# Kernel optimization log

Hardware: AMD Instinct MI355X
Metric: run time of the kernel (lower is better)

## Reference

```python
import jax, jax.numpy as jnp
import numpy as np

TOP_K = 2
EPS = float(np.finfo(np.float64).eps)  # combine() clamps zeros to np.finfo(float).eps


def setup_inputs() -> dict:
    key = jax.random.key(0)
    ks = jax.random.split(key, 6)
    B, D, H, O, E = 2048, 1024, 2048, 512, 8
    return {
        "x": jax.random.normal(ks[0], (B, D), dtype=jnp.float32),
        "w_gate": jax.random.normal(ks[1], (D, E), dtype=jnp.float32) * 0.02,
        "fc1_w": jax.random.normal(ks[2], (E, D, H), dtype=jnp.float32) * 0.02,
        "fc1_b": jax.random.normal(ks[3], (E, H), dtype=jnp.float32) * 0.02,
        "fc2_w": jax.random.normal(ks[4], (E, H, O), dtype=jnp.float32) * 0.02,
        "fc2_b": jax.random.normal(ks[5], (E, O), dtype=jnp.float32) * 0.02,
    }


def _gates(x, w_gate):
    # Noisy top-k gating in eval mode (no noise): clean logits -> top-k -> softmax over top-k -> scatter.
    logits = x @ w_gate                              # [B, E]
    top_logits, top_idx = jax.lax.top_k(logits, TOP_K)  # [B, K]
    top_gates = jax.nn.softmax(top_logits, axis=-1)      # 'softmax' gating over selected experts
    B = x.shape[0]
    gates = jnp.zeros(logits.shape, logits.dtype)
    gates = gates.at[jnp.arange(B)[:, None], top_idx].set(top_gates)
    return gates                                      # [B, E], zero for non-selected experts


def reference(x, w_gate, fc1_w, fc1_b, fc2_w, fc2_b):
    gates = _gates(x, w_gate)                         # [B, E]
    # Dense-equivalent of SparseDispatcher: non-selected experts have gate 0,
    # so weighting by gates reproduces dispatch/expert/combine exactly.
    h = jax.nn.gelu(jnp.einsum('bd,edh->ebh', x, fc1_w) + fc1_b[:, None, :],
                    approximate=False)                # [E, B, H]
    logp = jax.nn.log_softmax(jnp.einsum('ebh,eho->ebo', h, fc2_w) + fc2_b[:, None, :],
                              axis=-1)                # [E, B, O] (MLP ends with LogSoftmax)
    # combine: sum_e gates[b,e] * exp(logp_e[b]), clamp zeros to eps, then log
    combined = jnp.einsum('ebo,be->bo', jnp.exp(logp), gates)  # [B, O]
    combined = jnp.where(combined == 0, jnp.asarray(EPS, combined.dtype), combined)
    return jnp.log(combined)
```

## Files before the change

kernel.cpp:

```cpp
#include <hip/hip_runtime.h>
#include <stdint.h>

#define Bn 2048
#define Dn 1024
#define Hn 2048
#define On 512
#define En 8

typedef float f32x4 __attribute__((ext_vector_type(4)));
typedef unsigned short ushort_t;
typedef unsigned char u8;

__device__ __forceinline__ ushort_t f2bf(float v) {
  union { float f; uint32_t u; } a; a.f = v;
  uint32_t u = a.u;
  return (ushort_t)((u + 0x7fffu + ((u >> 16) & 1u)) >> 16);
}

__device__ __forceinline__ void gload16(const void* g, void* l) {
  __builtin_amdgcn_global_load_lds((const uint32_t*)g, (uint32_t*)l, 16, 0, 0);
}

__device__ __forceinline__ int pk4_fp8(float a, float b, float c, float d) {
  int w = __builtin_amdgcn_cvt_pk_fp8_f32(a, b, 0, false);
  w = __builtin_amdgcn_cvt_pk_fp8_f32(c, d, w, true);
  return w;
}

__device__ __forceinline__ u8 f2fp8(float v) {
  int w = __builtin_amdgcn_cvt_pk_fp8_f32(v, v, 0, false);
  return (u8)(w & 0xff);
}

__global__ void init_kernel(int* counts, int* cursors) {
  int t = threadIdx.x;
  if (t < En) { counts[t] = 0; cursors[t] = 0; }
}

__global__ __launch_bounds__(256) void cast_x8_kernel(const float* __restrict__ in,
                                                      u8* __restrict__ out) {
  int i = blockIdx.x * 256 + threadIdx.x;
  const float4* p = (const float4*)in + (size_t)i * 4;
  float4 a = p[0], b = p[1], c = p[2], d = p[3];
  int4 o;
  o.x = pk4_fp8(a.x, a.y, a.z, a.w);
  o.y = pk4_fp8(b.x, b.y, b.z, b.w);
  o.z = pk4_fp8(c.x, c.y, c.z, c.w);
  o.w = pk4_fp8(d.x, d.y, d.z, d.w);
  *(int4*)(out + (size_t)i * 16) = o;
}

#define NB_G (Bn / 8)
#define NB_T1 ((Dn / 64) * (Hn / 64) * En)
#define NB_T2 ((Hn / 64) * (On / 64) * En)
#define WSCALE 64.0f

__device__ __forceinline__ void tcast64_f8(const float* __restrict__ inp,
                                           u8* __restrict__ outp,
                                           int R, int C, int r0, int c0, float* tile) {
  int t = threadIdx.x;
  int rr = t >> 4, cc4 = (t & 15) * 4;
#pragma unroll
  for (int j = 0; j < 4; j++) {
    float4 v = *(const float4*)&inp[(size_t)(r0 + j * 16 + rr) * C + c0 + cc4];
    float* tp = &tile[(j * 16 + rr) * 65 + cc4];
    tp[0] = v.x; tp[1] = v.y; tp[2] = v.z; tp[3] = v.w;
  }
  __syncthreads();
  int orow = t >> 2, g = t & 3;
  int4 o;
#pragma unroll
  for (int q = 0; q < 4; q++) {
    float v0 = tile[(g * 16 + q * 4 + 0) * 65 + orow] * WSCALE;
    float v1 = tile[(g * 16 + q * 4 + 1) * 65 + orow] * WSCALE;
    float v2 = tile[(g * 16 + q * 4 + 2) * 65 + orow] * WSCALE;
    float v3 = tile[(g * 16 + q * 4 + 3) * 65 + orow] * WSCALE;
    ((int*)&o)[q] = pk4_fp8(v0, v1, v2, v3);
  }
  *(int4*)&outp[(size_t)(c0 + orow) * R + r0 + g * 16] = o;
}

__global__ __launch_bounds__(256) void prep_kernel(
    const float* __restrict__ x, const float* __restrict__ wg,
    const float* __restrict__ fc1w, const float* __restrict__ fc2w,
    u8* __restrict__ w1t8, u8* __restrict__ w2t8,
    int* __restrict__ top_idx, float* __restrict__ gates, int* __restrict__ counts) {
  __shared__ float smem[En * Dn];
  __shared__ int lcnt[En];
  int bid = blockIdx.x;
  int t = threadIdx.x;

  if (bid < NB_G) {
    float* wgs = smem;
    for (int i = t; i < Dn * En; i += 256) {
      int d = i >> 3, e = i & 7;
      wgs[e * Dn + d] = wg[i];
    }
    if (t < En) lcnt[t] = 0;
    __syncthreads();
    int w = t >> 6, lane = t & 63;
#pragma unroll
    for (int r = 0; r < 2; r++) {
      int b = bid * 8 + w * 2 + r;
      const float* xr = x + (size_t)b * Dn;
      float xv[16];
#pragma unroll
      for (int j = 0; j < 16; j++) xv[j] = xr[lane + j * 64];
      float acc[En];
#pragma unroll
      for (int e = 0; e < En; e++) acc[e] = 0.f;
#pragma unroll
      for (int j = 0; j < 16; j++) {
        int d = lane + j * 64;
#pragma unroll
        for (int e = 0; e < En; e++) acc[e] += xv[j] * wgs[e * Dn + d];
      }
#pragma unroll
      for (int off = 32; off; off >>= 1) {
#pragma unroll
        for (int e = 0; e < En; e++) acc[e] += __shfl_down(acc[e], off);
      }
      if (lane == 0) {
        float best = -1e30f, second = -1e30f; int bi = 0, si = 0;
#pragma unroll
        for (int e = 0; e < En; e++) {
          float l = acc[e];
          if (l > best) { second = best; si = bi; best = l; bi = e; }
          else if (l > second) { second = l; si = e; }
        }
        float e1 = expf(second - best);
        float inv = 1.f / (1.f + e1);
        top_idx[2 * b] = bi; top_idx[2 * b + 1] = si;
        gates[2 * b] = inv;  gates[2 * b + 1] = e1 * inv;
        atomicAdd(&lcnt[bi], 1);
        atomicAdd(&lcnt[si], 1);
      }
    }
    __syncthreads();
    if (t < En) {
      int c = lcnt[t];
      if (c) atomicAdd(&counts[t], c);
    }
  } else if (bid < NB_G + NB_T1) {
    int idx = bid - NB_G;
    constexpr int TPE = (Dn / 64) * (Hn / 64);
    int z = idx / TPE, rem = idx % TPE;
    int r0 = (rem / (Hn / 64)) * 64, c0 = (rem % (Hn / 64)) * 64;
    tcast64_f8(fc1w + (size_t)z * Dn * Hn, w1t8 + (size_t)z * Dn * Hn, Dn, Hn, r0, c0, smem);
  } else {
    int idx = bid - NB_G - NB_T1;
    constexpr int TPE = (Hn / 64) * (On / 64);
    int z = idx / TPE, rem = idx % TPE;
    int r0 = (rem / (On / 64)) * 64, c0 = (rem % (On / 64)) * 64;
    tcast64_f8(fc2w + (size_t)z * Hn * On, w2t8 + (size_t)z * Hn * On, Hn, On, r0, c0, smem);
  }
}

__global__ void offsets_kernel(const int* counts, int* offsets, int* cursors) {
  if (threadIdx.x == 0) {
    int s = 0;
    for (int e = 0; e < En; e++) { offsets[e] = s; s += counts[e]; }
  }
  if (threadIdx.x < En) cursors[threadIdx.x] = 0;
}

__global__ void assign_kernel(const int* __restrict__ top_idx, const int* __restrict__ offsets,
                              int* cursors, int* __restrict__ s2r, int* __restrict__ r2s) {
  int b = blockIdx.x * 256 + threadIdx.x;
  if (b >= Bn) return;
#pragma unroll
  for (int k = 0; k < 2; k++) {
    int e = top_idx[2 * b + k];
    int pos = atomicAdd(&cursors[e], 1);
    int slot = offsets[e] + pos;
    s2r[slot] = b;
    r2s[2 * b + k] = slot;
  }
}

template <bool FC1, int N, int K, int SPLITK>
__global__ __launch_bounds__(256, 8) void fp8_gemm_kernel(
    const u8* __restrict__ A, const u8* __restrict__ WT,
    const float* __restrict__ bias, const int* __restrict__ offsets,
    const int* __restrict__ counts, const int* __restrict__ s2r,
    u8* __restrict__ outH8, float* __restrict__ outL, float* __restrict__ outL2) {
  constexpr int NBL = N / 64;
  constexpr int KS = K / SPLITK;
  constexpr int NT = KS / 64;
  int e = blockIdx.z;
  int cnt = counts[e];
  int rb = blockIdx.y;
  if (rb * 64 >= cnt) return;
  int base = offsets[e];
  int ks = blockIdx.x / NBL;
  int nb = (blockIdx.x % NBL) * 64;
  int k0 = ks * KS;
  __shared__ __align__(16) u8 As[64 * 64];
  __shared__ __align__(16) u8 Bs[64 * 64];
  int t = threadIdx.x;
  int lane = t & 63, w = t >> 6;
  int wr = w >> 1, wc = w & 1;

  int srow = t >> 2;
  int sslot = (t & 3) ^ ((srow >> 1) & 3);
  int scol = sslot * 16;

  int lr = rb * 64 + srow;
  int lrc = lr < cnt ? lr : cnt - 1;
  const u8* aptr = A + (size_t)(FC1 ? s2r[base + lrc] : (base + lrc)) * K + k0 + scol;
  const u8* bptr = WT + ((size_t)e * N + nb + srow) * K + k0 + scol;

  f32x4 zero = {0.f, 0.f, 0.f, 0.f};
  f32x4 acc[2][2];
#pragma unroll
  for (int m = 0; m < 2; m++)
#pragma unroll
    for (int n = 0; n < 2; n++) acc[m][n] = zero;

  int a_r = wr * 32 + (lane & 15);
  int b_r = wc * 32 + (lane & 15);
  int rkey = ((lane & 15) >> 1) & 3;
  int slb = (lane >> 4) >> 1;
  int half = ((lane >> 4) & 1) * 8;

  for (int kt = 0; kt < NT; kt++) {
    gload16(aptr + kt * 64, &As[t * 16]);
    gload16(bptr + kt * 64, &Bs[t * 16]);
    __syncthreads();
#pragma unroll
    for (int kk = 0; kk < 2; kk++) {
      long af[2], bfr[2];
#pragma unroll
      for (int m = 0; m < 2; m++)
        af[m] = *(const long*)(As + (a_r + m * 16) * 64 +
                               (((kk * 2 + slb) ^ rkey) << 4) + half);
#pragma unroll
      for (int n = 0; n < 2; n++)
        bfr[n] = *(const long*)(Bs + (b_r + n * 16) * 64 +
                                (((kk * 2 + slb) ^ rkey) << 4) + half);
#pragma unroll
      for (int m = 0; m < 2; m++)
#pragma unroll
        for (int n = 0; n < 2; n++)
          acc[m][n] = __builtin_amdgcn_mfma_f32_16x16x32_fp8_fp8(af[m], bfr[n], acc[m][n], 0, 0, 0);
    }
    __syncthreads();
  }

  const float INV = 1.0f / WSCALE;
  float* dst = (SPLITK > 1 && ks > 0) ? outL2 : outL;
  int lr0 = rb * 64 + wr * 32;
#pragma unroll
  for (int m = 0; m < 2; m++) {
#pragma unroll
    for (int i = 0; i < 4; i++) {
      int orow = lr0 + m * 16 + (lane >> 4) * 4 + i;
      if (orow < cnt) {
        int slot = base + orow;
#pragma unroll
        for (int n = 0; n < 2; n++) {
          int col = nb + wc * 32 + n * 16 + (lane & 15);
          if (FC1) {
            float v = acc[m][n][i] * INV + bias[e * N + col];
            float g = 0.5f * v * (1.0f + erff(v * 0.70710678118654752f));
            outH8[(size_t)slot * N + col] = f2fp8(g);
          } else {
            float v = acc[m][n][i] * INV + (ks == 0 ? bias[e * N + col] : 0.f);
            dst[(size_t)slot * N + col] = v;
          }
        }
      }
    }
  }
}

__device__ __forceinline__ float blk_reduce(float v, bool ismax) {
  __shared__ float sbuf[4];
  int lane = threadIdx.x & 63, w = threadIdx.x >> 6;
#pragma unroll
  for (int off = 32; off; off >>= 1) {
    float o = __shfl_down(v, off);
    v = ismax ? fmaxf(v, o) : (v + o);
  }
  __syncthreads();
  if (lane == 0) sbuf[w] = v;
  __syncthreads();
  float r = sbuf[0];
#pragma unroll
  for (int i = 1; i < 4; i++) r = ismax ? fmaxf(r, sbuf[i]) : (r + sbuf[i]);
  return r;
}

__global__ void combine_kernel(const float* __restrict__ l2a, const float* __restrict__ l2b,
                               const int* __restrict__ r2s, const float* __restrict__ gates,
                               float* __restrict__ out) {
  int b = blockIdx.x, t = threadIdx.x;
  float c0 = 0.f, c1 = 0.f;
#pragma unroll
  for (int k = 0; k < 2; k++) {
    int slot = r2s[2 * b + k];
    float g = gates[2 * b + k];
    const float* lp0 = l2a + (size_t)slot * On;
    const float* lp1 = l2b + (size_t)slot * On;
    float v0 = lp0[t] + lp1[t];
    float v1 = lp0[t + 256] + lp1[t + 256];
    float m = blk_reduce(fmaxf(v0, v1), true);
    float s = blk_reduce(expf(v0 - m) + expf(v1 - m), false);
    float lse = m + logf(s);
    c0 += g * expf(v0 - lse);
    c1 += g * expf(v1 - lse);
  }
  const float EPSv = 2.220446049250313e-16f;
  out[(size_t)b * On + t] = logf(fmaxf(c0, EPSv));
  out[(size_t)b * On + t + 256] = logf(fmaxf(c1, EPSv));
}

extern "C" void kernel_launch(void* const* d_in, const int* in_sizes, int n_in,
                              void* d_out, int out_size, void* d_ws, size_t ws_size,
                              hipStream_t stream) {
  const float* x = (const float*)d_in[0];
  const float* wgate = (const float*)d_in[1];
  const float* fc1w = (const float*)d_in[2];
  const float* fc1b = (const float*)d_in[3];
  const float* fc2w = (const float*)d_in[4];
  const float* fc2b = (const float*)d_in[5];
  float* out = (float*)d_out;

  char* ws = (char*)d_ws;
  size_t o = 0;
  u8* x_f8     = (u8*)(ws + o);    o += (size_t)Bn * Dn;
  u8* w1t8     = (u8*)(ws + o);    o += (size_t)En * Hn * Dn;
  u8* w2t8     = (u8*)(ws + o);    o += (size_t)En * On * Hn;
  u8* hbuf8    = (u8*)(ws + o);    o += (size_t)2 * Bn * Hn;
  float* l2buf = (float*)(ws + o); o += (size_t)2 * Bn * On * 4;
  int* top_idx = (int*)(ws + o);   o += (size_t)Bn * 2 * 4;
  float* gates = (float*)(ws + o); o += (size_t)Bn * 2 * 4;
  int* r2s     = (int*)(ws + o);   o += (size_t)Bn * 2 * 4;
  int* s2r     = (int*)(ws + o);   o += (size_t)2 * Bn * 4;
  int* counts  = (int*)(ws + o);   o += 64;
  int* offsets = (int*)(ws + o);   o += 64;
  int* cursors = (int*)(ws + o);   o += 64;
  float* l2buf1 = (float*)w1t8;

  hipLaunchKernelGGL(init_kernel, dim3(1), dim3(64), 0, stream, counts, cursors);
  hipLaunchKernelGGL(cast_x8_kernel, dim3(Bn * Dn / 16 / 256), dim3(256), 0, stream, x, x_f8);
  hipLaunchKernelGGL(prep_kernel, dim3(NB_G + NB_T1 + NB_T2), dim3(256), 0, stream,
                     x, wgate, fc1w, fc2w, w1t8, w2t8, top_idx, gates, counts);
  hipLaunchKernelGGL(offsets_kernel, dim3(1), dim3(64), 0, stream, counts, offsets, cursors);
  hipLaunchKernelGGL(assign_kernel, dim3(Bn / 256), dim3(256), 0, stream,
                     top_idx, offsets, cursors, s2r, r2s);
  hipLaunchKernelGGL((fp8_gemm_kernel<true, Hn, Dn, 1>), dim3(Hn / 64, 32, En), dim3(256),
                     0, stream, x_f8, w1t8, fc1b, offsets, counts, s2r, hbuf8,
                     (float*)nullptr, (float*)nullptr);
  hipLaunchKernelGGL((fp8_gemm_kernel<false, On, Hn, 2>), dim3((On / 64) * 2, 32, En), dim3(256),
                     0, stream, hbuf8, w2t8, fc2b, offsets, counts, s2r, (u8*)nullptr,
                     l2buf, l2buf1);
  hipLaunchKernelGGL(combine_kernel, dim3(Bn), dim3(256), 0, stream, l2buf, l2buf1, r2s, gates, out);
}
```

Baseline: 115.2 us.

## Fuse x fp8 cast into prep kernel and convert weight tiles to fp8 before LDS transpose

Drops the separate x-cast launch and handles the x-to-fp8 conversion in extra blocks of the prep kernel. The weight transpose-cast now covers 256x64 tiles per block. It converts to fp8 in registers before writing to LDS, so the transpose moves bytes instead of floats and each thread writes 64-byte contiguous output rows. This cuts LDS traffic, block count and one launch, at the cost of more per-thread global loads and a larger per-block tile.

```diff
diff --git a/kernel.cpp b/kernel.cpp
--- a/kernel.cpp
+++ b/kernel.cpp
@@ -11,12 +11,6 @@
 typedef unsigned short ushort_t;
 typedef unsigned char u8;
 
-__device__ __forceinline__ ushort_t f2bf(float v) {
-  union { float f; uint32_t u; } a; a.f = v;
-  uint32_t u = a.u;
-  return (ushort_t)((u + 0x7fffu + ((u >> 16) & 1u)) >> 16);
-}
-
 __device__ __forceinline__ void gload16(const void* g, void* l) {
   __builtin_amdgcn_global_load_lds((const uint32_t*)g, (uint32_t*)l, 16, 0, 0);
 }
@@ -37,53 +31,52 @@
   if (t < En) { counts[t] = 0; cursors[t] = 0; }
 }
 
-__global__ __launch_bounds__(256) void cast_x8_kernel(const float* __restrict__ in,
-                                                      u8* __restrict__ out) {
-  int i = blockIdx.x * 256 + threadIdx.x;
-  const float4* p = (const float4*)in + (size_t)i * 4;
-  float4 a = p[0], b = p[1], c = p[2], d = p[3];
-  int4 o;
-  o.x = pk4_fp8(a.x, a.y, a.z, a.w);
-  o.y = pk4_fp8(b.x, b.y, b.z, b.w);
-  o.z = pk4_fp8(c.x, c.y, c.z, c.w);
-  o.w = pk4_fp8(d.x, d.y, d.z, d.w);
-  *(int4*)(out + (size_t)i * 16) = o;
-}
-
 #define NB_G (Bn / 8)
-#define NB_T1 ((Dn / 64) * (Hn / 64) * En)
-#define NB_T2 ((Hn / 64) * (On / 64) * En)
+#define NB_T1 ((Dn / 256) * (Hn / 64) * En)
+#define NB_T2 ((Hn / 256) * (On / 64) * En)
+#define NB_X (Bn * Dn / 4096)
 #define WSCALE 64.0f
 
-__device__ __forceinline__ void tcast64_f8(const float* __restrict__ inp,
-                                           u8* __restrict__ outp,
-                                           int R, int C, int r0, int c0, float* tile) {
+__device__ __forceinline__ void tcast_f8_256(const float* __restrict__ inp,
+                                             u8* __restrict__ outp,
+                                             int R, int C, int r0, int c0, u8* lds) {
   int t = threadIdx.x;
-  int rr = t >> 4, cc4 = (t & 15) * 4;
-#pragma unroll
-  for (int j = 0; j < 4; j++) {
-    float4 v = *(const float4*)&inp[(size_t)(r0 + j * 16 + rr) * C + c0 + cc4];
-    float* tp = &tile[(j * 16 + rr) * 65 + cc4];
-    tp[0] = v.x; tp[1] = v.y; tp[2] = v.z; tp[3] = v.w;
+  int cc4 = (t & 15) * 4;
+  int rr4 = (t >> 4) * 4;
+#pragma unroll
+  for (int pass = 0; pass < 4; pass++) {
+    int rbase = pass * 64 + rr4;
+    uint32_t wds[4] = {0, 0, 0, 0};
+#pragma unroll
+    for (int i = 0; i < 4; i++) {
+      float4 v = *(const float4*)&inp[(size_t)(r0 + rbase + i) * C + c0 + cc4];
+      wds[0] |= (uint32_t)f2fp8(v.x * WSCALE) << (8 * i);
+      wds[1] |= (uint32_t)f2fp8(v.y * WSCALE) << (8 * i);
+      wds[2] |= (uint32_t)f2fp8(v.z * WSCALE) << (8 * i);
+      wds[3] |= (uint32_t)f2fp8(v.w * WSCALE) << (8 * i);
+    }
+#pragma unroll
+    for (int j = 0; j < 4; j++)
+      *(uint32_t*)&lds[(cc4 + j) * 272 + rbase] = wds[j];
   }
   __syncthreads();
-  int orow = t >> 2, g = t & 3;
-  int4 o;
-#pragma unroll
-  for (int q = 0; q < 4; q++) {
-    float v0 = tile[(g * 16 + q * 4 + 0) * 65 + orow] * WSCALE;
-    float v1 = tile[(g * 16 + q * 4 + 1) * 65 + orow] * WSCALE;
-    float v2 = tile[(g * 16 + q * 4 + 2) * 65 + orow] * WSCALE;
-    float v3 = tile[(g * 16 + q * 4 + 3) * 65 + orow] * WSCALE;
-    ((int*)&o)[q] = pk4_fp8(v0, v1, v2, v3);
-  }
-  *(int4*)&outp[(size_t)(c0 + orow) * R + r0 + g * 16] = o;
+  int j = t >> 2, q = t & 3;
+  const u8* lp = &lds[j * 272 + q * 64];
+  int4 d0 = *(const int4*)(lp);
+  int4 d1 = *(const int4*)(lp + 16);
+  int4 d2 = *(const int4*)(lp + 32);
+  int4 d3 = *(const int4*)(lp + 48);
+  u8* op = &outp[(size_t)(c0 + j) * R + r0 + q * 64];
+  *(int4*)(op) = d0;
+  *(int4*)(op + 16) = d1;
+  *(int4*)(op + 32) = d2;
+  *(int4*)(op + 48) = d3;
 }
 
 __global__ __launch_bounds__(256) void prep_kernel(
     const float* __restrict__ x, const float* __restrict__ wg,
     const float* __restrict__ fc1w, const float* __restrict__ fc2w,
-    u8* __restrict__ w1t8, u8* __restrict__ w2t8,
+    u8* __restrict__ x_f8, u8* __restrict__ w1t8, u8* __restrict__ w2t8,
     int* __restrict__ top_idx, float* __restrict__ gates, int* __restrict__ counts) {
   __shared__ float smem[En * Dn];
   __shared__ int lcnt[En];
@@ -143,16 +136,28 @@
     }
   } else if (bid < NB_G + NB_T1) {
     int idx = bid - NB_G;
-    constexpr int TPE = (Dn / 64) * (Hn / 64);
+    constexpr int TPE = (Dn / 256) * (Hn / 64);
     int z = idx / TPE, rem = idx % TPE;
-    int r0 = (rem / (Hn / 64)) * 64, c0 = (rem % (Hn / 64)) * 64;
-    tcast64_f8(fc1w + (size_t)z * Dn * Hn, w1t8 + (size_t)z * Dn * Hn, Dn, Hn, r0, c0, smem);
+    int r0 = (rem / (Hn / 64)) * 256, c0 = (rem % (Hn / 64)) * 64;
+    tcast_f8_256(fc1w + (size_t)z * Dn * Hn, w1t8 + (size_t)z * Dn * Hn, Dn, Hn, r0, c0,
+                 (u8*)smem);
+  } else if (bid < NB_G + NB_T1 + NB_T2) {
+    int idx = bid - NB_G - NB_T1;
+    constexpr int TPE = (Hn / 256) * (On / 64);
+    int z = idx / TPE, rem = idx % TPE;
+    int r0 = (rem / (On / 64)) * 256, c0 = (rem % (On / 64)) * 64;
+    tcast_f8_256(fc2w + (size_t)z * Hn * On, w2t8 + (size_t)z * Hn * On, Hn, On, r0, c0,
+                 (u8*)smem);
   } else {
-    int idx = bid - NB_G - NB_T1;
-    constexpr int TPE = (Hn / 64) * (On / 64);
-    int z = idx / TPE, rem = idx % TPE;
-    int r0 = (rem / (On / 64)) * 64, c0 = (rem % (On / 64)) * 64;
-    tcast64_f8(fc2w + (size_t)z * Hn * On, w2t8 + (size_t)z * Hn * On, Hn, On, r0, c0, smem);
+    int i = (bid - NB_G - NB_T1 - NB_T2) * 256 + t;
+    const float4* p = (const float4*)x + (size_t)i * 4;
+    float4 a = p[0], b = p[1], c = p[2], d = p[3];
+    int4 o;
+    o.x = pk4_fp8(a.x, a.y, a.z, a.w);
+    o.y = pk4_fp8(b.x, b.y, b.z, b.w);
+    o.z = pk4_fp8(c.x, c.y, c.z, c.w);
+    o.w = pk4_fp8(d.x, d.y, d.z, d.w);
+    *(int4*)(x_f8 + (size_t)i * 16) = o;
   }
 }
 
@@ -343,9 +348,8 @@
   float* l2buf1 = (float*)w1t8;
 
   hipLaunchKernelGGL(init_kernel, dim3(1), dim3(64), 0, stream, counts, cursors);
-  hipLaunchKernelGGL(cast_x8_kernel, dim3(Bn * Dn / 16 / 256), dim3(256), 0, stream, x, x_f8);
-  hipLaunchKernelGGL(prep_kernel, dim3(NB_G + NB_T1 + NB_T2), dim3(256), 0, stream,
-                     x, wgate, fc1w, fc2w, w1t8, w2t8, top_idx, gates, counts);
+  hipLaunchKernelGGL(prep_kernel, dim3(NB_G + NB_T1 + NB_T2 + NB_X), dim3(256), 0, stream,
+                     x, wgate, fc1w, fc2w, x_f8, w1t8, w2t8, top_idx, gates, counts);
   hipLaunchKernelGGL(offsets_kernel, dim3(1), dim3(64), 0, stream, counts, offsets, cursors);
   hipLaunchKernelGGL(assign_kernel, dim3(Bn / 256), dim3(256), 0, stream,
                      top_idx, offsets, cursors, s2r, r2s);
```

After: 115.6 us. About the same (+0.3%).
